# Kernel tuning notes

Measured on AMD Instinct MI355X. Metric: run time of the kernel, lower is better.

The kernel has to match this reference:

```python
import jax, jax.numpy as jnp
import numpy as np

N_CLS, N_YAW, NY, NX, DOF = 3, 2, 160, 160, 7
N_BOXES = 32
IOU_THRESH = [(0.45, 0.60), (0.35, 0.50), (0.35, 0.50)]
ALLOW_LOW_QUALITY = True
EPS = 1e-8
BEV_COLS = np.array([0, 1, 3, 4, 6])  # x, y, w, l, yaw


def _cross(a, b):
    return a[..., 0] * b[..., 1] - a[..., 1] * b[..., 0]


def _corners(b):
    # b: [5] (x, y, w, l, yaw) -> [4, 2] rectangle corners
    c, s = jnp.cos(b[4]), jnp.sin(b[4])
    u = jnp.stack([c, s]) * (b[2] * 0.5)
    v = jnp.stack([-s, c]) * (b[3] * 0.5)
    ctr = b[:2]
    return jnp.stack([ctr + u + v, ctr + u - v, ctr - u - v, ctr - u + v])


def _inside(pts, b):
    # pts: [4,2] in rotated rect b: [5] -> [4] bool
    c, s = jnp.cos(b[4]), jnp.sin(b[4])
    rel = pts - b[:2]
    du = rel[:, 0] * c + rel[:, 1] * s
    dv = -rel[:, 0] * s + rel[:, 1] * c
    return (jnp.abs(du) <= b[2] * 0.5 + 1e-5) & (jnp.abs(dv) <= b[3] * 0.5 + 1e-5)


def _pair_iou(b1, b2):
    # exact rotated-rect IoU via convex intersection polygon (candidate points + angular sort + shoelace)
    c1, c2 = _corners(b1), _corners(b2)
    m1, m2 = _inside(c1, b2), _inside(c2, b1)
    d1 = jnp.roll(c1, -1, 0) - c1
    d2 = jnp.roll(c2, -1, 0) - c2
    qp = c2[None, :, :] - c1[:, None, :]              # [4,4,2]
    den = _cross(d1[:, None, :], d2[None, :, :])       # [4,4]
    den_safe = jnp.where(jnp.abs(den) < EPS, 1.0, den)
    t = _cross(qp, d2[None, :, :]) / den_safe
    s = _cross(qp, d1[:, None, :]) / den_safe
    ok = (jnp.abs(den) >= EPS) & (t >= 0) & (t <= 1) & (s >= 0) & (s <= 1)
    ipts = c1[:, None, :] + t[..., None] * d1[:, None, :]
    pts = jnp.concatenate([c1, c2, ipts.reshape(16, 2)])   # [24,2] candidates
    mask = jnp.concatenate([m1, m2, ok.reshape(16)])
    nv = mask.sum()
    ctr = (pts * mask[:, None]).sum(0) / jnp.maximum(nv, 1)
    ang = jnp.arctan2(pts[:, 1] - ctr[1], pts[:, 0] - ctr[0])
    order = jnp.argsort(jnp.where(mask, ang, 1e9))          # valid points first, CCW
    p = pts[order]
    p = jnp.where(jnp.arange(24)[:, None] < nv, p, p[0])    # pad tail with first vertex
    nxt = jnp.roll(p, -1, 0)
    inter = 0.5 * jnp.abs(jnp.sum(p[:, 0] * nxt[:, 1] - nxt[:, 0] * p[:, 1]))
    union = b1[2] * b1[3] + b2[2] * b2[3] - inter
    return jnp.clip(inter / jnp.maximum(union, EPS), 0.0, 1.0)


def _box_iou_rotated(boxes, anchors):
    # boxes [G,5], anchors [A,5] -> [G,A]
    return jax.vmap(lambda b: jax.vmap(lambda a: _pair_iou(b, a))(anchors))(boxes)


def _match(iou, valid_gt, low, high):
    # detectron2-style Matcher with labels [0, -1, +1]
    matched_vals = iou.max(0)
    matches = iou.argmax(0)
    labels = jnp.where(matched_vals >= high, 1, jnp.where(matched_vals >= low, -1, 0))
    if ALLOW_LOW_QUALITY:
        highest = iou.max(1)  # best IoU per gt
        best = (iou == highest[:, None]) & valid_gt[:, None] & (highest > 0)[:, None]
        labels = jnp.where(best.any(0), 1, labels)
    return matches, labels


def reference(boxes, anchors, class_idx):
    n_cls, n_yaw, ny, nx, dof = anchors.shape
    bev = boxes[:, BEV_COLS]
    matches_l, labels_l = [], []
    for i in range(n_cls):  # small fixed class loop, as in the original
        anch_i = anchors[i].reshape(-1, dof)
        iou = _box_iou_rotated(bev, anch_i[:, BEV_COLS])
        valid = class_idx == i
        # boxes of other classes masked to -1 (equivalent to the boolean-gather per-class loop)
        iou = jax.lax.stop_gradient(jnp.where(valid[:, None], iou, -1.0))
        low, high = IOU_THRESH[i]
        m, lab = _match(iou, valid, low, high)
        matches_l.append(m.reshape(n_yaw, ny, nx))
        labels_l.append(lab.reshape(n_yaw, ny, nx))
    box_idx = jnp.stack(matches_l)   # [n_cls,n_yaw,ny,nx] global gt index
    labels = jnp.stack(labels_l)
    # --- handle_assignment_conflicts (in-place torch ops -> functional where) ---
    ambiguous = (labels == 1).sum(0) > 1
    labels = jnp.where(ambiguous[None], -1, labels)
    negative = (labels == 0).any(0)
    positive = (labels == 1).sum(0) == 1
    labels = jnp.where((negative & ~positive)[None], 0, labels)
    loss_mask = ~(labels == -1).all(0, keepdims=True)
    labels = jnp.where(labels == -1, 0, labels)
    # --- get_reg_targets (VoxelNet encoding), computed dense then masked ---
    G = boxes[box_idx]  # [n_cls,n_yaw,ny,nx,7]
    norm = jnp.linalg.norm(anchors[..., 3:5], axis=-1, keepdims=True)
    a_norm = jnp.concatenate([norm, norm, anchors[..., 5:6]], -1)
    vals = jnp.concatenate([
        (G[..., :3] - anchors[..., :3]) / a_norm,
        jnp.log(G[..., 3:6] / anchors[..., 3:6]),
        G[..., 6:7] - anchors[..., 6:7]], -1)
    G_reg = jnp.where((labels == 1)[..., None], vals, 0.0)
    M_reg = labels[:, :-1, :, :, None].sum(1, keepdims=True).astype(jnp.float32)
    G_cls = labels.astype(jnp.float32)
    M_cls = loss_mask.astype(jnp.float32)
    return G_cls, G_reg, M_cls, M_reg


def setup_inputs() -> dict:
    key = jax.random.key(0)
    ks = jax.random.split(key, 6)
    sizes = jnp.array([[1.6, 3.9, 1.56], [0.6, 0.8, 1.73], [0.76, 1.76, 1.73]])  # w,l,h per class
    z_ctr = jnp.array([-1.0, -0.6, -0.6])
    xs = jnp.linspace(0.32, 70.08, NX)
    ys = jnp.linspace(-39.8, 39.8, NY)
    yaws = jnp.array([0.0, np.pi / 2])
    shp = (N_CLS, N_YAW, NY, NX)
    gx = jnp.broadcast_to(xs[None, None, None, :], shp)
    gy = jnp.broadcast_to(ys[None, None, :, None], shp)
    gz = jnp.broadcast_to(z_ctr[:, None, None, None], shp)
    gwlh = jnp.broadcast_to(sizes[:, None, None, None, :], shp + (3,))
    gyaw = jnp.broadcast_to(yaws[None, :, None, None], shp)
    anchors = jnp.concatenate([jnp.stack([gx, gy, gz], -1), gwlh, gyaw[..., None]], -1)
    class_idx = jax.random.randint(ks[0], (N_BOXES,), 0, N_CLS)
    x = jax.random.uniform(ks[1], (N_BOXES,), minval=0.0, maxval=70.4)
    y = jax.random.uniform(ks[2], (N_BOXES,), minval=-40.0, maxval=40.0)
    z = z_ctr[class_idx] + 0.1 * jax.random.normal(ks[3], (N_BOXES,))
    wlh = sizes[class_idx] * jax.random.uniform(ks[4], (N_BOXES, 3), minval=0.85, maxval=1.15)
    yaw = jax.random.uniform(ks[5], (N_BOXES,), minval=-np.pi, maxval=np.pi)
    boxes = jnp.concatenate([jnp.stack([x, y, z], -1), wlh, yaw[:, None]], -1)
    return {"boxes": boxes, "anchors": anchors, "class_idx": class_idx}
```

## Files before the change

### kernel.cpp

```cpp
#include <hip/hip_runtime.h>
#include <math.h>

#define NCLS 3
#define NYAW 2
#define NYG 160
#define NXG 160
#define NB 32
#define NANCH (NYAW * NYG * NXG)
#define DOF 7
#define EPSI 1e-8f

#define OFF_GCLS 0
#define OFF_GREG (NCLS * NANCH)
#define OFF_MCLS (OFF_GREG + NCLS * NANCH * DOF)
#define OFF_MREG (OFF_MCLS + NANCH)

struct BBev { float x, y, w, l, yaw; };

__device__ __forceinline__ float crossv(float ax, float ay, float bx, float by) {
    return ax * by - ay * bx;
}

__device__ float pair_iou(const BBev b1, const BBev b2) {
    float ddx = b1.x - b2.x, ddy = b1.y - b2.y;
    float r1 = 0.5f * sqrtf(b1.w * b1.w + b1.l * b1.l);
    float r2 = 0.5f * sqrtf(b2.w * b2.w + b2.l * b2.l);
    float rr = r1 + r2 + 1e-3f;
    if (ddx * ddx + ddy * ddy > rr * rr) return 0.0f;

    float cs1 = cosf(b1.yaw), sn1 = sinf(b1.yaw);
    float cs2 = cosf(b2.yaw), sn2 = sinf(b2.yaw);

    float c1x[4], c1y[4], c2x[4], c2y[4];
    {
        float ux = cs1 * (b1.w * 0.5f), uy = sn1 * (b1.w * 0.5f);
        float vx = -sn1 * (b1.l * 0.5f), vy = cs1 * (b1.l * 0.5f);
        c1x[0] = b1.x + ux + vx; c1y[0] = b1.y + uy + vy;
        c1x[1] = b1.x + ux - vx; c1y[1] = b1.y + uy - vy;
        c1x[2] = b1.x - ux - vx; c1y[2] = b1.y - uy - vy;
        c1x[3] = b1.x - ux + vx; c1y[3] = b1.y - uy + vy;
    }
    {
        float ux = cs2 * (b2.w * 0.5f), uy = sn2 * (b2.w * 0.5f);
        float vx = -sn2 * (b2.l * 0.5f), vy = cs2 * (b2.l * 0.5f);
        c2x[0] = b2.x + ux + vx; c2y[0] = b2.y + uy + vy;
        c2x[1] = b2.x + ux - vx; c2y[1] = b2.y + uy - vy;
        c2x[2] = b2.x - ux - vx; c2y[2] = b2.y - uy - vy;
        c2x[3] = b2.x - ux + vx; c2y[3] = b2.y - uy + vy;
    }

    float qx[24], qy[24];
    int n = 0;

    for (int i = 0; i < 4; i++) {
        float rx = c1x[i] - b2.x, ry = c1y[i] - b2.y;
        float du = rx * cs2 + ry * sn2;
        float dv = -rx * sn2 + ry * cs2;
        if (fabsf(du) <= b2.w * 0.5f + 1e-5f && fabsf(dv) <= b2.l * 0.5f + 1e-5f) {
            qx[n] = c1x[i]; qy[n] = c1y[i]; n++;
        }
    }
    for (int i = 0; i < 4; i++) {
        float rx = c2x[i] - b1.x, ry = c2y[i] - b1.y;
        float du = rx * cs1 + ry * sn1;
        float dv = -rx * sn1 + ry * cs1;
        if (fabsf(du) <= b1.w * 0.5f + 1e-5f && fabsf(dv) <= b1.l * 0.5f + 1e-5f) {
            qx[n] = c2x[i]; qy[n] = c2y[i]; n++;
        }
    }
    for (int i = 0; i < 4; i++) {
        float d1x = c1x[(i + 1) & 3] - c1x[i];
        float d1y = c1y[(i + 1) & 3] - c1y[i];
        for (int j = 0; j < 4; j++) {
            float d2x = c2x[(j + 1) & 3] - c2x[j];
            float d2y = c2y[(j + 1) & 3] - c2y[j];
            float den = crossv(d1x, d1y, d2x, d2y);
            if (fabsf(den) < EPSI) continue;
            float qpx = c2x[j] - c1x[i], qpy = c2y[j] - c1y[i];
            float t = crossv(qpx, qpy, d2x, d2y) / den;
            float s = crossv(qpx, qpy, d1x, d1y) / den;
            if (t >= 0.0f && t <= 1.0f && s >= 0.0f && s <= 1.0f) {
                qx[n] = c1x[i] + t * d1x;
                qy[n] = c1y[i] + t * d1y;
                n++;
            }
        }
    }

    float inter = 0.0f;
    if (n > 0) {
        float sx = 0.0f, sy = 0.0f;
        for (int k = 0; k < n; k++) { sx += qx[k]; sy += qy[k]; }
        float cx = sx / (float)n, cy = sy / (float)n;

        float ang[24];
        for (int k = 0; k < n; k++) ang[k] = atan2f(qy[k] - cy, qx[k] - cx);

        for (int k = 1; k < n; k++) {
            float a = ang[k], x = qx[k], y = qy[k];
            int m = k - 1;
            while (m >= 0 && ang[m] > a) {
                ang[m + 1] = ang[m]; qx[m + 1] = qx[m]; qy[m + 1] = qy[m];
                m--;
            }
            ang[m + 1] = a; qx[m + 1] = x; qy[m + 1] = y;
        }

        float area = 0.0f;
        for (int k = 0; k < n; k++) {
            int kn = (k + 1 == n) ? 0 : k + 1;
            area += qx[k] * qy[kn] - qx[kn] * qy[k];
        }
        inter = 0.5f * fabsf(area);
    }

    float uni = b1.w * b1.l + b2.w * b2.l - inter;
    float iou = inter / fmaxf(uni, EPSI);
    return fminf(fmaxf(iou, 0.0f), 1.0f);
}

__global__ void iou_kernel(const float* __restrict__ boxes,
                           const float* __restrict__ anchors,
                           const int* __restrict__ cls,
                           float* __restrict__ iou_mat,
                           float* __restrict__ maxval,
                           int* __restrict__ argmax,
                           float* __restrict__ highest) {
    __shared__ BBev sb[NB];
    __shared__ int scls[NB];
    int tid = threadIdx.x;
    if (tid < NB) {
        const float* bp = boxes + tid * DOF;
        sb[tid].x = bp[0]; sb[tid].y = bp[1];
        sb[tid].w = bp[3]; sb[tid].l = bp[4];
        sb[tid].yaw = bp[6];
        scls[tid] = cls[tid];
    }
    __syncthreads();

    int idx = blockIdx.x * blockDim.x + tid;
    if (idx >= NCLS * NANCH) return;
    int c = idx / NANCH;
    int a = idx - c * NANCH;

    const float* ap = anchors + (size_t)idx * DOF;
    BBev ab;
    ab.x = ap[0]; ab.y = ap[1]; ab.w = ap[3]; ab.l = ap[4]; ab.yaw = ap[6];

    float best = -INFINITY;
    int bidx = 0;
    for (int b = 0; b < NB; b++) {
        float val = -1.0f;
        if (scls[b] == c) {
            val = pair_iou(sb[b], ab);
            if (val > 0.0f) {
                atomicMax((int*)&highest[c * NB + b], __float_as_int(val));
            }
        }
        iou_mat[((size_t)(c * NB + b)) * NANCH + a] = val;
        if (val > best) { best = val; bidx = b; }
    }
    maxval[idx] = best;
    argmax[idx] = bidx;
}

__global__ void label_kernel(const float* __restrict__ iou_mat,
                             const float* __restrict__ maxval,
                             const float* __restrict__ highest,
                             const int* __restrict__ cls,
                             int* __restrict__ labels) {
    int idx = blockIdx.x * blockDim.x + threadIdx.x;
    if (idx >= NCLS * NANCH) return;
    int c = idx / NANCH;
    int a = idx - c * NANCH;

    float low  = (c == 0) ? 0.45f : 0.35f;
    float high = (c == 0) ? 0.60f : 0.50f;
    float mv = maxval[idx];
    int lab = (mv >= high) ? 1 : ((mv >= low) ? -1 : 0);

    if (lab != 1) {
        for (int b = 0; b < NB; b++) {
            if (cls[b] == c) {
                float h = highest[c * NB + b];
                if (h > 0.0f && iou_mat[((size_t)(c * NB + b)) * NANCH + a] == h) {
                    lab = 1;
                    break;
                }
            }
        }
    }
    labels[idx] = lab;
}

__global__ void out_kernel(const float* __restrict__ boxes,
                           const float* __restrict__ anchors,
                           const int* __restrict__ labels_in,
                           const int* __restrict__ argmax,
                           float* __restrict__ out) {
    int s = blockIdx.x * blockDim.x + threadIdx.x;
    if (s >= NANCH) return;

    int lab[NCLS];
    for (int c = 0; c < NCLS; c++) lab[c] = labels_in[c * NANCH + s];

    int pos = 0;
    for (int c = 0; c < NCLS; c++) pos += (lab[c] == 1);
    if (pos > 1) { for (int c = 0; c < NCLS; c++) lab[c] = -1; }

    bool neg = false; pos = 0;
    for (int c = 0; c < NCLS; c++) { neg |= (lab[c] == 0); pos += (lab[c] == 1); }
    if (neg && pos != 1) { for (int c = 0; c < NCLS; c++) lab[c] = 0; }

    bool lm = false;
    for (int c = 0; c < NCLS; c++) lm |= (lab[c] != -1);

    float* G_cls = out + OFF_GCLS;
    float* G_reg = out + OFF_GREG;
    float* M_cls = out + OFF_MCLS;
    float* M_reg = out + OFF_MREG;

    M_cls[s] = lm ? 1.0f : 0.0f;

    for (int c = 0; c < NCLS; c++) {
        int L = (lab[c] == -1) ? 0 : lab[c];
        G_cls[c * NANCH + s] = (float)L;
        if (s < NYG * NXG) M_reg[c * (NYG * NXG) + s] = (float)L;

        float v0 = 0.f, v1 = 0.f, v2 = 0.f, v3 = 0.f, v4 = 0.f, v5 = 0.f, v6 = 0.f;
        if (L == 1) {
            const float* A = anchors + ((size_t)(c * NANCH + s)) * DOF;
            const float* G = boxes + (size_t)argmax[c * NANCH + s] * DOF;
            float nrm = sqrtf(A[3] * A[3] + A[4] * A[4]);
            v0 = (G[0] - A[0]) / nrm;
            v1 = (G[1] - A[1]) / nrm;
            v2 = (G[2] - A[2]) / A[5];
            v3 = logf(G[3] / A[3]);
            v4 = logf(G[4] / A[4]);
            v5 = logf(G[5] / A[5]);
            v6 = G[6] - A[6];
        }
        size_t rb = ((size_t)(c * NANCH + s)) * DOF;
        G_reg[rb + 0] = v0; G_reg[rb + 1] = v1; G_reg[rb + 2] = v2;
        G_reg[rb + 3] = v3; G_reg[rb + 4] = v4; G_reg[rb + 5] = v5;
        G_reg[rb + 6] = v6;
    }
}

extern "C" void kernel_launch(void* const* d_in, const int* in_sizes, int n_in,
                              void* d_out, int out_size, void* d_ws, size_t ws_size,
                              hipStream_t stream) {
    const float* boxes   = (const float*)d_in[0];
    const float* anchors = (const float*)d_in[1];
    const int*   cls     = (const int*)d_in[2];
    float* out = (float*)d_out;

    char* ws = (char*)d_ws;
    float* iou_mat = (float*)(ws);
    float* maxval  = (float*)(ws + 19660800);
    int*   argmax  = (int*)  (ws + 20275200);
    int*   labels  = (int*)  (ws + 20889600);
    float* highest = (float*)(ws + 21504000);

    hipMemsetAsync(highest, 0, NCLS * NB * sizeof(float), stream);

    iou_kernel<<<dim3((NCLS * NANCH) / 256), dim3(256), 0, stream>>>(
        boxes, anchors, cls, iou_mat, maxval, argmax, highest);
    label_kernel<<<dim3((NCLS * NANCH) / 256), dim3(256), 0, stream>>>(
        iou_mat, maxval, highest, cls, labels);
    out_kernel<<<dim3(NANCH / 256), dim3(256), 0, stream>>>(
        boxes, anchors, labels, argmax, out);
}
```

Measured before the change: 52.87 us.

## Fuse IoU, labeling and target kernels into one cooperative grid-synced kernel

Replaces the three-kernel pipeline and memset with a single cooperative kernel. Each thread handles one anchor position and computes IoU against only the boxes of that box's class, cutting per-anchor IoU work by about the number of classes. Per-anchor IoUs stay in shared memory instead of a large global IoU matrix. A grid sync separates the global per-box max reduction from labeling. This removes global IoU/label traffic and launch overhead, but adds two grid-wide barriers, a large shared-memory footprint that limits occupancy, and requires all 200 blocks to be co-resident.

```diff
diff --git a/kernel.cpp b/kernel.cpp
--- a/kernel.cpp
+++ b/kernel.cpp
@@ -1,5 +1,8 @@
 #include <hip/hip_runtime.h>
+#include <hip/hip_cooperative_groups.h>
 #include <math.h>
+
+namespace cg = cooperative_groups;
 
 #define NCLS 3
 #define NYAW 2
@@ -9,6 +12,8 @@
 #define NANCH (NYAW * NYG * NXG)
 #define DOF 7
 #define EPSI 1e-8f
+#define NTHREADS 256
+#define NBLOCKS (NANCH / NTHREADS)
 
 #define OFF_GCLS 0
 #define OFF_GREG (NCLS * NANCH)
@@ -97,13 +102,13 @@
         for (int k = 0; k < n; k++) ang[k] = atan2f(qy[k] - cy, qx[k] - cx);
 
         for (int k = 1; k < n; k++) {
-            float a = ang[k], x = qx[k], y = qy[k];
+            float aa = ang[k], x = qx[k], y = qy[k];
             int m = k - 1;
-            while (m >= 0 && ang[m] > a) {
+            while (m >= 0 && ang[m] > aa) {
                 ang[m + 1] = ang[m]; qx[m + 1] = qx[m]; qy[m + 1] = qy[m];
                 m--;
             }
-            ang[m + 1] = a; qx[m + 1] = x; qy[m + 1] = y;
+            ang[m + 1] = aa; qx[m + 1] = x; qy[m + 1] = y;
         }
 
         float area = 0.0f;
@@ -119,100 +124,103 @@
     return fminf(fmaxf(iou, 0.0f), 1.0f);
 }
 
-__global__ void iou_kernel(const float* __restrict__ boxes,
-                           const float* __restrict__ anchors,
-                           const int* __restrict__ cls,
-                           float* __restrict__ iou_mat,
-                           float* __restrict__ maxval,
-                           int* __restrict__ argmax,
-                           float* __restrict__ highest) {
-    __shared__ BBev sb[NB];
+__global__ void __launch_bounds__(NTHREADS)
+fused_kernel(const float* __restrict__ boxes,
+             const float* __restrict__ anchors,
+             const int* __restrict__ cls,
+             float* __restrict__ out,
+             float* __restrict__ highest) {
+    __shared__ float sbx[NB], sby[NB], sbw[NB], sbl[NB], sbyaw[NB];
     __shared__ int scls[NB];
+    __shared__ float shigh[NB];
+    __shared__ float siou[NTHREADS][NB + 1];
+
     int tid = threadIdx.x;
+    int a = blockIdx.x * NTHREADS + tid;
+
     if (tid < NB) {
         const float* bp = boxes + tid * DOF;
-        sb[tid].x = bp[0]; sb[tid].y = bp[1];
-        sb[tid].w = bp[3]; sb[tid].l = bp[4];
-        sb[tid].yaw = bp[6];
+        sbx[tid] = bp[0]; sby[tid] = bp[1];
+        sbw[tid] = bp[3]; sbl[tid] = bp[4];
+        sbyaw[tid] = bp[6];
         scls[tid] = cls[tid];
     }
+    if (blockIdx.x == 0 && tid < NB) highest[tid] = 0.0f;
     __syncthreads();
 
-    int idx = blockIdx.x * blockDim.x + tid;
-    if (idx >= NCLS * NANCH) return;
-    int c = idx / NANCH;
-    int a = idx - c * NANCH;
-
-    const float* ap = anchors + (size_t)idx * DOF;
-    BBev ab;
-    ab.x = ap[0]; ab.y = ap[1]; ab.w = ap[3]; ab.l = ap[4]; ab.yaw = ap[6];
-
-    float best = -INFINITY;
-    int bidx = 0;
+    cg::grid_group grid = cg::this_grid();
+    grid.sync();
+
+    float ax   = anchors[(size_t)a * DOF + 0];
+    float ay   = anchors[(size_t)a * DOF + 1];
+    float ayaw = anchors[(size_t)a * DOF + 6];
+    float aw0 = anchors[((size_t)(0 * NANCH) + a) * DOF + 3];
+    float al0 = anchors[((size_t)(0 * NANCH) + a) * DOF + 4];
+    float aw1 = anchors[((size_t)(1 * NANCH) + a) * DOF + 3];
+    float al1 = anchors[((size_t)(1 * NANCH) + a) * DOF + 4];
+    float aw2 = anchors[((size_t)(2 * NANCH) + a) * DOF + 3];
+    float al2 = anchors[((size_t)(2 * NANCH) + a) * DOF + 4];
+
+    float best0 = -1.0f, best1 = -1.0f, best2 = -1.0f;
+    int arg0 = 0, arg1 = 0, arg2 = 0;
+
+#pragma unroll 1
     for (int b = 0; b < NB; b++) {
-        float val = -1.0f;
-        if (scls[b] == c) {
-            val = pair_iou(sb[b], ab);
-            if (val > 0.0f) {
-                atomicMax((int*)&highest[c * NB + b], __float_as_int(val));
-            }
-        }
-        iou_mat[((size_t)(c * NB + b)) * NANCH + a] = val;
-        if (val > best) { best = val; bidx = b; }
-    }
-    maxval[idx] = best;
-    argmax[idx] = bidx;
-}
-
-__global__ void label_kernel(const float* __restrict__ iou_mat,
-                             const float* __restrict__ maxval,
-                             const float* __restrict__ highest,
-                             const int* __restrict__ cls,
-                             int* __restrict__ labels) {
-    int idx = blockIdx.x * blockDim.x + threadIdx.x;
-    if (idx >= NCLS * NANCH) return;
-    int c = idx / NANCH;
-    int a = idx - c * NANCH;
-
-    float low  = (c == 0) ? 0.45f : 0.35f;
-    float high = (c == 0) ? 0.60f : 0.50f;
-    float mv = maxval[idx];
-    int lab = (mv >= high) ? 1 : ((mv >= low) ? -1 : 0);
-
-    if (lab != 1) {
-        for (int b = 0; b < NB; b++) {
-            if (cls[b] == c) {
-                float h = highest[c * NB + b];
-                if (h > 0.0f && iou_mat[((size_t)(c * NB + b)) * NANCH + a] == h) {
-                    lab = 1;
-                    break;
+        int c = scls[b];
+        BBev bb; bb.x = sbx[b]; bb.y = sby[b]; bb.w = sbw[b]; bb.l = sbl[b]; bb.yaw = sbyaw[b];
+        BBev ab; ab.x = ax; ab.y = ay;
+        ab.w = (c == 0) ? aw0 : ((c == 1) ? aw1 : aw2);
+        ab.l = (c == 0) ? al0 : ((c == 1) ? al1 : al2);
+        ab.yaw = ayaw;
+        float v = pair_iou(bb, ab);
+        siou[tid][b] = v;
+        if (v > 0.0f) atomicMax((int*)(highest + b), __float_as_int(v));
+        if (c == 0)      { if (v > best0) { best0 = v; arg0 = b; } }
+        else if (c == 1) { if (v > best1) { best1 = v; arg1 = b; } }
+        else             { if (v > best2) { best2 = v; arg2 = b; } }
+    }
+
+    grid.sync();
+
+    if (tid < NB) shigh[tid] = highest[tid];
+    __syncthreads();
+
+    int lab[NCLS];
+#pragma unroll
+    for (int c = 0; c < NCLS; c++) {
+        float mv   = (c == 0) ? best0 : ((c == 1) ? best1 : best2);
+        float low  = (c == 0) ? 0.45f : 0.35f;
+        float high = (c == 0) ? 0.60f : 0.50f;
+        int L = (mv >= high) ? 1 : ((mv >= low) ? -1 : 0);
+        if (L != 1) {
+            for (int b = 0; b < NB; b++) {
+                if (scls[b] == c) {
+                    float h = shigh[b];
+                    if (h > 0.0f && siou[tid][b] == h) { L = 1; break; }
                 }
             }
         }
-    }
-    labels[idx] = lab;
-}
-
-__global__ void out_kernel(const float* __restrict__ boxes,
-                           const float* __restrict__ anchors,
-                           const int* __restrict__ labels_in,
-                           const int* __restrict__ argmax,
-                           float* __restrict__ out) {
-    int s = blockIdx.x * blockDim.x + threadIdx.x;
-    if (s >= NANCH) return;
-
-    int lab[NCLS];
-    for (int c = 0; c < NCLS; c++) lab[c] = labels_in[c * NANCH + s];
+        lab[c] = L;
+    }
 
     int pos = 0;
+#pragma unroll
     for (int c = 0; c < NCLS; c++) pos += (lab[c] == 1);
-    if (pos > 1) { for (int c = 0; c < NCLS; c++) lab[c] = -1; }
+    if (pos > 1) {
+#pragma unroll
+        for (int c = 0; c < NCLS; c++) lab[c] = -1;
+    }
 
     bool neg = false; pos = 0;
+#pragma unroll
     for (int c = 0; c < NCLS; c++) { neg |= (lab[c] == 0); pos += (lab[c] == 1); }
-    if (neg && pos != 1) { for (int c = 0; c < NCLS; c++) lab[c] = 0; }
+    if (neg && pos != 1) {
+#pragma unroll
+        for (int c = 0; c < NCLS; c++) lab[c] = 0;
+    }
 
     bool lm = false;
+#pragma unroll
     for (int c = 0; c < NCLS; c++) lm |= (lab[c] != -1);
 
     float* G_cls = out + OFF_GCLS;
@@ -220,17 +228,19 @@
     float* M_cls = out + OFF_MCLS;
     float* M_reg = out + OFF_MREG;
 
-    M_cls[s] = lm ? 1.0f : 0.0f;
-
+    M_cls[a] = lm ? 1.0f : 0.0f;
+
+#pragma unroll
     for (int c = 0; c < NCLS; c++) {
         int L = (lab[c] == -1) ? 0 : lab[c];
-        G_cls[c * NANCH + s] = (float)L;
-        if (s < NYG * NXG) M_reg[c * (NYG * NXG) + s] = (float)L;
+        G_cls[c * NANCH + a] = (float)L;
+        if (a < NYG * NXG) M_reg[c * (NYG * NXG) + a] = (float)L;
 
         float v0 = 0.f, v1 = 0.f, v2 = 0.f, v3 = 0.f, v4 = 0.f, v5 = 0.f, v6 = 0.f;
         if (L == 1) {
-            const float* A = anchors + ((size_t)(c * NANCH + s)) * DOF;
-            const float* G = boxes + (size_t)argmax[c * NANCH + s] * DOF;
+            int am = (c == 0) ? arg0 : ((c == 1) ? arg1 : arg2);
+            const float* A = anchors + ((size_t)(c * NANCH + a)) * DOF;
+            const float* G = boxes + (size_t)am * DOF;
             float nrm = sqrtf(A[3] * A[3] + A[4] * A[4]);
             v0 = (G[0] - A[0]) / nrm;
             v1 = (G[1] - A[1]) / nrm;
@@ -240,7 +250,7 @@
             v5 = logf(G[5] / A[5]);
             v6 = G[6] - A[6];
         }
-        size_t rb = ((size_t)(c * NANCH + s)) * DOF;
+        size_t rb = ((size_t)(c * NANCH + a)) * DOF;
         G_reg[rb + 0] = v0; G_reg[rb + 1] = v1; G_reg[rb + 2] = v2;
         G_reg[rb + 3] = v3; G_reg[rb + 4] = v4; G_reg[rb + 5] = v5;
         G_reg[rb + 6] = v6;
@@ -254,20 +264,10 @@
     const float* anchors = (const float*)d_in[1];
     const int*   cls     = (const int*)d_in[2];
     float* out = (float*)d_out;
-
-    char* ws = (char*)d_ws;
-    float* iou_mat = (float*)(ws);
-    float* maxval  = (float*)(ws + 19660800);
-    int*   argmax  = (int*)  (ws + 20275200);
-    int*   labels  = (int*)  (ws + 20889600);
-    float* highest = (float*)(ws + 21504000);
-
-    hipMemsetAsync(highest, 0, NCLS * NB * sizeof(float), stream);
-
-    iou_kernel<<<dim3((NCLS * NANCH) / 256), dim3(256), 0, stream>>>(
-        boxes, anchors, cls, iou_mat, maxval, argmax, highest);
-    label_kernel<<<dim3((NCLS * NANCH) / 256), dim3(256), 0, stream>>>(
-        iou_mat, maxval, highest, cls, labels);
-    out_kernel<<<dim3(NANCH / 256), dim3(256), 0, stream>>>(
-        boxes, anchors, labels, argmax, out);
-}
+    float* highest = (float*)d_ws;
+
+    void* args[] = { (void*)&boxes, (void*)&anchors, (void*)&cls,
+                     (void*)&out, (void*)&highest };
+    hipLaunchCooperativeKernel((void*)fused_kernel, dim3(NBLOCKS), dim3(NTHREADS),
+                               args, 0, stream);
+}
```

Measured after the change: 88.05 us. 66.5% more time.
